# Optimization experiments

Measured on AMD Instinct MI355X. Metric: run time of the kernel, lower is better.

## Reference

```python
import jax, jax.numpy as jnp
from jax import lax
import numpy as np


def _conv(x, w, stride):
    # x: [B,C,D,H,W], w: [3,3,3,Cin,Cout]; kernel 3, pad 1 (matches SubMConv3d / SparseConv3d(3, s, padding=1))
    return lax.conv_general_dilated(x, w, (stride, stride, stride), [(1, 1)] * 3,
                                    dimension_numbers=('NCDHW', 'DHWIO', 'NCDHW'))


def _bn_relu(y, scale, shift, mask):
    # eval-mode BatchNorm folded to scale/shift, ReLU, then restrict to active sites
    return jnp.maximum(y * scale[None, :, None, None, None] + shift[None, :, None, None, None], 0.0) * mask


def _downsample_mask(m):
    # SparseConv3d(k=3, s=2, p=1): output site active iff any input in its 3x3x3 window is active
    return lax.reduce_window(m, -jnp.inf, lax.max, (1, 1, 3, 3, 3), (1, 1, 2, 2, 2),
                             [(0, 0), (0, 0), (1, 1), (1, 1), (1, 1)])


def setup_inputs() -> dict:
    key = jax.random.key(0)
    ks = jax.random.split(key, 40)
    B, D = 1, 128
    occ = jax.random.uniform(ks[0], (B, 1, D, D, D)) < 0.05
    x = jax.random.normal(ks[1], (B, 16, D, D, D), jnp.float32) * occ

    def w(k, ci, co):
        return jax.random.normal(k, (3, 3, 3, ci, co), jnp.float32) * (1.0 / np.sqrt(27.0 * ci))

    def sc(k, c):
        return jax.random.uniform(k, (c,), jnp.float32, 0.5, 1.5)

    def sh(k, c):
        return jax.random.normal(k, (c,), jnp.float32) * 0.1

    chans = [(16, 16), (16, 16), (16, 32), (32, 32), (32, 32), (32, 64), (64, 64), (64, 64), (64, 64)]
    names = ['w0a', 'w0b', 'wd0', 'w1a', 'w1b', 'wd1', 'w2a', 'w2b', 'w2c']
    d = {'x': x, 'mask': occ}
    i = 2
    for n, (ci, co) in zip(names, chans):
        d[n] = w(ks[i], ci, co)
        d['s' + n[1:]] = sc(ks[i + 1], co)
        d['b' + n[1:]] = sh(ks[i + 2], co)
        i += 3
    return d


def reference(x, mask, w0a, s0a, b0a, w0b, s0b, b0b, wd0, sd0, bd0,
              w1a, s1a, b1a, w1b, s1b, b1b, wd1, sd1, bd1,
              w2a, s2a, b2a, w2b, s2b, b2b, w2c, s2c, b2c):
    m0 = mask.astype(x.dtype)                       # active sites at full res [B,1,128,128,128]
    h = _bn_relu(_conv(x, w0a, 1), s0a, b0a, m0)    # conv0 (subm0)
    h = _bn_relu(_conv(h, w0b, 1), s0b, b0b, m0)
    m1 = _downsample_mask(m0)                       # down0 activity [B,1,64,64,64]
    h = _bn_relu(_conv(h, wd0, 2), sd0, bd0, m1)
    h = _bn_relu(_conv(h, w1a, 1), s1a, b1a, m1)    # conv1 (subm1)
    h = _bn_relu(_conv(h, w1b, 1), s1b, b1b, m1)
    m2 = _downsample_mask(m1)                       # down1 activity [B,1,32,32,32]
    h = _bn_relu(_conv(h, wd1, 2), sd1, bd1, m2)
    h = _bn_relu(_conv(h, w2a, 1), s2a, b2a, m2)    # conv2 (subm2)
    h = _bn_relu(_conv(h, w2b, 1), s2b, b2b, m2)
    h = _bn_relu(_conv(h, w2c, 1), s2c, b2c, m2)
    return h                                        # .dense() -> [B,64,32,32,32]
```

## Files before the change

### kernel.cpp

```cpp
#include <hip/hip_runtime.h>
#include <cstdint>

typedef unsigned short u16;
typedef unsigned int u32;
typedef unsigned char u8;
typedef unsigned long long u64;
typedef __attribute__((ext_vector_type(8))) short short8;
typedef __attribute__((ext_vector_type(4))) float f32x4;

#define CAP 131072

__device__ __forceinline__ float bf1(u16 v){ union{u32 i; float f;} c; c.i = ((u32)v) << 16; return c.f; }
__device__ __forceinline__ u16 f2bf(float f){
    union{float f; u32 i;} c; c.f = f; u32 i = c.i;
    return (u16)((i + 0x7FFFu + ((i >> 16) & 1u)) >> 16);
}
__device__ __forceinline__ u16 bits2bf(u32 b){ union{u32 i; float f;} c; c.i = b; return f2bf(c.f); }

struct PAll {
    const void* w[9];
    u32 wstart[10];
    int cin[9], cout[9], mode[9];
    const void* s[18];
};

__global__ __launch_bounds__(256)
void prepact_k(PAll J, u16* __restrict__ FR, float* __restrict__ S,
               const u16* __restrict__ s0a_probe, u32* __restrict__ flag,
               const void* __restrict__ xv, u64* __restrict__ bmask,
               u32* __restrict__ cnt, u16* __restrict__ Xp){
    int ok = 1;
    #pragma unroll
    for (int i = 0; i < 8; i += 2){
        u16 vv = s0a_probe[i];
        if (vv < 0x3F00u || vv > 0x3FC0u) ok = 0;
    }
    const u32 isbf = ok ? 1u : 0u;

    if (blockIdx.x < 8192){
        const int v = blockIdx.x * 256 + threadIdx.x;
        const size_t N = 2097152;
        u16 vals[16];
        u32 a = 0;
        if (isbf) {
            const u16* x = (const u16*)xv;
            #pragma unroll
            for (int c = 0; c < 16; ++c){
                const u16 b = x[(size_t)c * N + v];
                vals[c] = b;
                a |= (u32)b & 0x7FFFu;
            }
        } else {
            const u32* x = (const u32*)xv;
            #pragma unroll
            for (int c = 0; c < 16; ++c){
                const u32 b = x[(size_t)c * N + v];
                vals[c] = bits2bf(b);
                a |= b & 0x7FFFFFFFu;
            }
        }
        const bool act = (a != 0);
        const u64 m = __ballot(act);
        __shared__ u32 wc[4];
        const int lane = threadIdx.x & 63, wv = threadIdx.x >> 6;
        if (lane == 0) { bmask[v >> 6] = m; wc[wv] = (u32)__popcll(m); }
        __syncthreads();
        if (act){
            u32 wbase = 0;
            for (int i = 0; i < wv; ++i) wbase += wc[i];
            const u32 local = wbase + (u32)__popcll(m & ((1ull << lane) - 1ull));
            u16* dst = Xp + ((size_t)blockIdx.x * 256 + local) * 16;
            *(short8*)(dst)     = *(const short8*)(vals);
            *(short8*)(dst + 8) = *(const short8*)(vals + 8);
        }
        return;
    }

    const int gi = (int)(blockIdx.x - 8192) * 256 + threadIdx.x;
    if (gi == 0) { flag[0] = isbf; cnt[0] = 0; }

    const int wtot = (int)J.wstart[9];
    if (gi < wtot){
        int j = 0;
        while (gi >= (int)J.wstart[j + 1]) ++j;
        const int i = gi - (int)J.wstart[j];
        const void* w = J.w[j];
        const int CIN = J.cin[j], COUT = J.cout[j];
        const int jj = i & 7;
        const int lane = (i >> 3) & 63;
        int rest = i >> 9;
        int src = -1;
        if (J.mode[j] == 0){
            const int KC = CIN >> 5, NT = COUT >> 4;
            const int nt = rest % NT; rest /= NT;
            const int kc = rest % KC; const int tap = rest / KC;
            const int k = kc * 32 + (lane >> 4) * 8 + jj;
            const int co = nt * 16 + (lane & 15);
            src = (tap * CIN + k) * COUT + co;
        } else if (J.mode[j] == 1){
            const int nt = rest & 1; const int pair = rest >> 1;
            const int kg = (lane >> 4) * 8 + jj;
            const int tap = pair * 2 + (kg >> 4);
            const int ci = kg & 15;
            const int co = nt * 16 + (lane & 15);
            if (tap < 27) src = (tap * 16 + ci) * 32 + co;
        } else {
            const int pair = rest;
            const int kg = (lane >> 4) * 8 + jj;
            const int tap = pair * 2 + (kg >> 4);
            const int ci = kg & 15;
            const int co = lane & 15;
            if (tap < 27) src = (tap * 16 + ci) * 16 + co;
        }
        float v = 0.f;
        if (src >= 0) v = isbf ? bf1(((const u16*)w)[src]) : ((const float*)w)[src];
        FR[gi] = f2bf(v);
    } else {
        const int i2 = gi - wtot;
        const int len[18] = {16,16,16,16,32,32,32,32,32,32,64,64,64,64,64,64,64,64};
        const int off[18] = {0,16,32,48,64,96,128,160,192,224,256,320,384,448,512,576,640,704};
        if (i2 < 768){
            int b = 0, base = 0;
            while (i2 >= base + len[b]) { base += len[b]; ++b; }
            const int t = i2 - base;
            const float v = isbf ? bf1(((const u16*)J.s[b])[t]) : ((const float*)J.s[b])[t];
            S[off[b] + t] = v;
        }
    }
}

__global__ __launch_bounds__(256)
void scatter2m_k(const u16* __restrict__ Xp, const u64* __restrict__ bmask,
                 int* __restrict__ idxmap, int* __restrict__ alist,
                 u16* __restrict__ f, u32* __restrict__ cnt,
                 u8* __restrict__ m1, u8* __restrict__ m2){
    if (blockIdx.x < 512){
        const int lane = threadIdx.x & 63, wv = threadIdx.x >> 6;
        __shared__ u32 wcnt[16][4];
        __shared__ u32 tileoff[16];
        __shared__ u32 sbase;
        const int tile0 = blockIdx.x * 16;

        #pragma unroll
        for (int i = 0; i < 16; ++i){
            if (lane == 0){
                const u64 m = bmask[(size_t)(tile0 + i) * 4 + wv];
                wcnt[i][wv] = (u32)__popcll(m);
            }
        }
        __syncthreads();
        if (threadIdx.x == 0){
            u32 s = 0;
            #pragma unroll
            for (int i = 0; i < 16; ++i){
                tileoff[i] = s;
                s += wcnt[i][0] + wcnt[i][1] + wcnt[i][2] + wcnt[i][3];
            }
            sbase = atomicAdd(cnt, s);
        }
        __syncthreads();
        const u32 b0 = sbase;
        #pragma unroll
        for (int i = 0; i < 16; ++i){
            const u64 m = bmask[(size_t)(tile0 + i) * 4 + wv];
            const bool act = (m >> lane) & 1ull;
            u32 wbase = 0;
            for (int k = 0; k < wv; ++k) wbase += wcnt[i][k];
            const u32 rank = (u32)__popcll(m & ((1ull << lane) - 1ull));
            const int v = (tile0 + i) * 256 + threadIdx.x;
            int slot = -1;
            if (act){
                const u32 sl = b0 + tileoff[i] + wbase + rank;
                if (sl < CAP){
                    slot = (int)sl;
                    alist[slot] = v;
                    const u16* src = Xp + ((size_t)(tile0 + i) * 256 + wbase + rank) * 16;
                    u16* dst = f + (size_t)slot * 16;
                    *(short8*)(dst)     = *(const short8*)(src);
                    *(short8*)(dst + 8) = *(const short8*)(src + 8);
                }
            }
            idxmap[v] = slot;
        }
    } else if (blockIdx.x < 1536){
        const int v = (int)(blockIdx.x - 512) * 256 + threadIdx.x;
        const int xo = v & 63, yo = (v >> 6) & 63, zo = v >> 12;
        u32 a = 0;
        #pragma unroll
        for (int kz = 0; kz < 3; ++kz){ const int iz = 2*zo + kz - 1; if ((unsigned)iz >= 128u) continue;
          #pragma unroll
          for (int ky = 0; ky < 3; ++ky){ const int iy = 2*yo + ky - 1; if ((unsigned)iy >= 128u) continue;
            #pragma unroll
            for (int kx = 0; kx < 3; ++kx){ const int ix = 2*xo + kx - 1; if ((unsigned)ix >= 128u) continue;
              const int vv = (iz * 128 + iy) * 128 + ix;
              a |= (u32)((bmask[vv >> 6] >> (vv & 63)) & 1ull);
        }}}
        m1[v] = (u8)a;
    } else {
        const int v = (int)(blockIdx.x - 1536) * 256 + threadIdx.x;
        const int xo = v & 31, yo = (v >> 5) & 31, zo = v >> 10;
        const int xlo = max(0, 4*xo - 3), xhi = min(127, 4*xo + 3);
        const int w0 = xlo >> 6, w1 = xhi >> 6;
        u32 a = 0;
        #pragma unroll
        for (int dz = -3; dz <= 3; ++dz){ const int iz = 4*zo + dz; if ((unsigned)iz >= 128u) continue;
          #pragma unroll
          for (int dy = -3; dy <= 3; ++dy){ const int iy = 4*yo + dy; if ((unsigned)iy >= 128u) continue;
            const int rowword = ((iz * 128 + iy) * 128) >> 6;
            if (w0 == w1){
                const u64 mw = bmask[rowword + w0];
                const int sh = xlo & 63, len = xhi - xlo + 1;
                if ((mw >> sh) & ((1ull << len) - 1ull)) a = 1;
            } else {
                const u64 lo = bmask[rowword + w0] >> (xlo & 63);
                const u64 hi = bmask[rowword + w1] & ((1ull << ((xhi & 63) + 1)) - 1ull);
                if (lo | hi) a = 1;
            }
        }}
        m2[v] = (u8)a;
    }
}

__global__ __launch_bounds__(256)
void sconvm_k(const u16* __restrict__ fin, const int* __restrict__ idxmap,
              const int* __restrict__ alist, const u32* __restrict__ cnt,
              const u16* __restrict__ wf, const float* __restrict__ sc,
              const float* __restrict__ sh, u16* __restrict__ fout){
    const int n = min((int)cnt[0], CAP);
    const int j = blockIdx.x * 4 + (threadIdx.x >> 6);
    const int sbase = j * 16;
    if (sbase >= n) return;
    const int lane = threadIdx.x & 63;
    const int m = lane & 15, quad = lane >> 4;

    const int s = sbase + m;
    const int v = (s < n) ? alist[s] : -1;
    int xo = 0, yo = 0, zo = 0;
    if (v >= 0){ xo = v & 127; yo = (v >> 7) & 127; zo = v >> 14; }

    f32x4 acc = {0.f,0.f,0.f,0.f};
    #pragma unroll
    for (int p = 0; p < 14; ++p){
        const int tp = p * 2 + (quad >> 1);
        short8 a = {0,0,0,0,0,0,0,0};
        if (v >= 0 && tp < 27){
            const int kz = tp / 9, ky = (tp / 3) % 3, kx = tp % 3;
            const int iz = zo + kz - 1, iy = yo + ky - 1, ix = xo + kx - 1;
            if ((unsigned)iz < 128u && (unsigned)iy < 128u && (unsigned)ix < 128u){
                const int sn = idxmap[((size_t)iz * 128 + iy) * 128 + ix];
                if (sn >= 0) a = *(const short8*)(fin + (size_t)sn * 16 + (quad & 1) * 8);
            }
        }
        short8 b = *(const short8*)(wf + ((size_t)p * 64 + lane) * 8);
        acc = __builtin_amdgcn_mfma_f32_16x16x32_bf16(a, b, acc, 0, 0, 0);
    }

    const int co = lane & 15;
    const float scl = sc[co], shf = sh[co];
    #pragma unroll
    for (int r = 0; r < 4; ++r){
        const int srow = sbase + quad * 4 + r;
        if (srow < n){
            fout[(size_t)srow * 16 + co] = f2bf(fmaxf(acc[r] * scl + shf, 0.f));
        }
    }
}

__global__ __launch_bounds__(256)
void convd0m_k(const u16* __restrict__ fbuf, const int* __restrict__ idxmap,
               const u16* __restrict__ wf, const float* __restrict__ sc,
               const float* __restrict__ sh, const u8* __restrict__ mk,
               u16* __restrict__ out)
{
    const int wj = blockIdx.x * 4 + (threadIdx.x >> 6);
    const int lane = threadIdx.x & 63;
    const int m = lane & 15, quad = lane >> 4;
    const int xo_b = (wj & 3) * 16;
    const int yo = (wj >> 2) & 63;
    const int zo = wj >> 8;

    f32x4 acc0 = {0.f,0.f,0.f,0.f}, acc1 = {0.f,0.f,0.f,0.f};
    const int ix_m = (xo_b + m) * 2 - 1;

    #pragma unroll
    for (int p = 0; p < 14; ++p){
        const int tp = p * 2 + (quad >> 1);
        short8 a = {0,0,0,0,0,0,0,0};
        if (tp < 27){
            const int kz = tp / 9, ky = (tp / 3) % 3, kx = tp % 3;
            const int iz = 2*zo + kz - 1, iy = 2*yo + ky - 1, ix = ix_m + kx;
            if ((unsigned)iz < 128u && (unsigned)iy < 128u && (unsigned)ix < 128u){
                const int sn = idxmap[((size_t)iz * 128 + iy) * 128 + ix];
                if (sn >= 0) a = *(const short8*)(fbuf + (size_t)sn * 16 + (quad & 1) * 8);
            }
        }
        short8 b0 = *(const short8*)(wf + ((size_t)(p*2+0) * 64 + lane) * 8);
        short8 b1 = *(const short8*)(wf + ((size_t)(p*2+1) * 64 + lane) * 8);
        acc0 = __builtin_amdgcn_mfma_f32_16x16x32_bf16(a, b0, acc0, 0, 0, 0);
        acc1 = __builtin_amdgcn_mfma_f32_16x16x32_bf16(a, b1, acc1, 0, 0, 0);
    }

    const int vb = wj * 16 + quad * 4;
    const u32 m4 = *(const u32*)(mk + vb);
    const int n = lane & 15;
    #pragma unroll
    for (int nt = 0; nt < 2; ++nt){
        const int co = nt * 16 + n;
        const float s = sc[co], h = sh[co];
        const f32x4 acc = nt ? acc1 : acc0;
        #pragma unroll
        for (int r = 0; r < 4; ++r){
            float val = fmaxf(acc[r] * s + h, 0.f);
            val = ((m4 >> (8*r)) & 0xFFu) ? val : 0.f;
            out[(size_t)(vb + r) * 32 + co] = f2bf(val);
        }
    }
}

template<int DIN, int DOUT, int CIN, int COUT, int STRIDE, int NSPLIT, bool FINAL>
__global__ __launch_bounds__(256)
void mconv_k(const u16* __restrict__ in, const u16* __restrict__ wf,
             const float* __restrict__ sc, const float* __restrict__ sh,
             const u8* __restrict__ mk, void* __restrict__ out,
             const u32* __restrict__ flag)
{
    constexpr int KC = CIN / 32;
    constexpr int NT = COUT / 16;
    constexpr int NTE = NT / NSPLIT;
    constexpr int XT = DOUT / 16;
    const int wjj = blockIdx.x * 4 + (threadIdx.x >> 6);
    const int cs = wjj % NSPLIT;
    const int wj = wjj / NSPLIT;
    const int lane = threadIdx.x & 63;
    const int m = lane & 15, quad = lane >> 4;

    const int xo_b = (wj % XT) * 16;
    const int yo = (wj / XT) % DOUT;
    const int zo = wj / (XT * DOUT);

    f32x4 acc[NTE];
    #pragma unroll
    for (int i = 0; i < NTE; ++i) acc[i] = (f32x4){0.f,0.f,0.f,0.f};

    const int ix0 = (xo_b + m) * STRIDE - 1;
    for (int kz = 0; kz < 3; ++kz){
      const int iz = zo * STRIDE + kz - 1;
      if ((unsigned)iz >= (unsigned)DIN) continue;
      for (int ky = 0; ky < 3; ++ky){
        const int iy = yo * STRIDE + ky - 1;
        if ((unsigned)iy >= (unsigned)DIN) continue;
        const size_t rowb = ((size_t)iz * DIN + iy) * DIN;
        #pragma unroll
        for (int kx = 0; kx < 3; ++kx){
          const int ix = ix0 + kx;
          const bool v = (unsigned)ix < (unsigned)DIN;
          const int tap = (kz*3 + ky)*3 + kx;
          const u16* ap = in + (rowb + ix) * CIN + quad * 8;
          const u16* bp = wf + (size_t)tap * KC * NT * 512 + lane * 8;
          #pragma unroll
          for (int kc = 0; kc < KC; ++kc){
            short8 a = {0,0,0,0,0,0,0,0};
            if (v) a = *(const short8*)(ap + kc * 32);
            #pragma unroll
            for (int nt = 0; nt < NTE; ++nt){
              short8 b = *(const short8*)(bp + (kc * NT + cs * NTE + nt) * 512);
              acc[nt] = __builtin_amdgcn_mfma_f32_16x16x32_bf16(a, b, acc[nt], 0, 0, 0);
            }
          }
    }}}

    const int vb = wj * 16 + quad * 4;
    const u32 m4 = *(const u32*)(mk + vb);
    const int n = lane & 15;
    #pragma unroll
    for (int nt = 0; nt < NTE; ++nt){
        const int co = (cs * NTE + nt) * 16 + n;
        const float s = sc[co], h = sh[co];
        #pragma unroll
        for (int r = 0; r < 4; ++r){
            float val = fmaxf(acc[nt][r] * s + h, 0.f);
            val = ((m4 >> (8*r)) & 0xFFu) ? val : 0.f;
            ((u16*)out)[(size_t)(vb + r) * COUT + co] = f2bf(val);
        }
    }
    (void)flag;
}

template<int D, int CIN, int COUT, int CSPLIT, bool FINAL>
__global__ __launch_bounds__((D/32)*4*64*CSPLIT)
void mconvw_k(const u16* __restrict__ in, const u16* __restrict__ wf,
              const float* __restrict__ sc, const float* __restrict__ sh,
              const u8* __restrict__ mk, void* __restrict__ out,
              const u32* __restrict__ flag)
{
    constexpr int KC = CIN / 32;
    constexpr int NT = COUT / 16;
    constexpr int NTE = NT / CSPLIT;
    constexpr int CH8 = CIN / 8;
    constexpr int WPR = D / 32;
    constexpr int BT = WPR * 4 * 64 * CSPLIT;
    __shared__ u16 tile[16 * 2048];

    const int t = threadIdx.x;
    const int yp = blockIdx.x % (D / 2);
    const int zp = blockIdx.x / (D / 2);

    #pragma unroll
    for (int ri = 0; ri < 16; ++ri){
        const int dz = ri >> 2, jy = ri & 3;
        const int iz = 2*zp + dz - 1, iy = 2*yp + jy - 1;
        if ((unsigned)iz < (unsigned)D && (unsigned)iy < (unsigned)D){
            const u16* src = in + ((size_t)(iz * D + iy) * D) * CIN;
            u16* dst = &tile[ri * 2048];
            for (int c = t; c < D * CH8; c += BT){
                const int x = c / CH8, c8 = c % CH8;
                *(short8*)(dst + (c8 * D + x) * 8) = *(const short8*)(src + c * 8);
            }
        }
    }
    __syncthreads();

    const int lane = t & 63, w = t >> 6;
    const int cs = w % CSPLIT;
    const int w2 = w / CSPLIT;
    const int r = w2 / WPR;
    const int r2z = r >> 1, r2y = r & 1;
    const int xo_b = (w2 % WPR) * 32;
    const int zo = 2*zp + r2z, yo = 2*yp + r2y;
    const int m = lane & 15, quad = lane >> 4;

    f32x4 acc0[NTE], acc1[NTE];
    #pragma unroll
    for (int i = 0; i < NTE; ++i){ acc0[i] = (f32x4){0.f,0.f,0.f,0.f}; acc1[i] = (f32x4){0.f,0.f,0.f,0.f}; }

    #pragma unroll
    for (int kz = 0; kz < 3; ++kz){
      const int iz = zo + kz - 1;
      if ((unsigned)iz >= (unsigned)D) continue;
      #pragma unroll
      for (int ky = 0; ky < 3; ++ky){
        const int iy = yo + ky - 1;
        if ((unsigned)iy >= (unsigned)D) continue;
        const u16* row = &tile[((r2z + kz) * 4 + (r2y + ky)) * 2048];
        #pragma unroll
        for (int kx = 0; kx < 3; ++kx){
          const int ix0 = xo_b + m + kx - 1;
          const int ix1 = ix0 + 16;
          const bool aok0 = (unsigned)ix0 < (unsigned)D;
          const bool aok1 = (unsigned)ix1 < (unsigned)D;
          const int tap = (kz * 3 + ky) * 3 + kx;
          const u16* bp = wf + (size_t)tap * KC * NT * 512 + lane * 8;
          #pragma unroll
          for (int kc = 0; kc < KC; ++kc){
            short8 a0 = {0,0,0,0,0,0,0,0};
            short8 a1 = {0,0,0,0,0,0,0,0};
            if (aok0) a0 = *(const short8*)(row + ((kc * 4 + quad) * D + ix0) * 8);
            if (aok1) a1 = *(const short8*)(row + ((kc * 4 + quad) * D + ix1) * 8);
            #pragma unroll
            for (int nt = 0; nt < NTE; ++nt){
              short8 b = *(const short8*)(bp + (kc * NT + cs * NTE + nt) * 512);
              acc0[nt] = __builtin_amdgcn_mfma_f32_16x16x32_bf16(a0, b, acc0[nt], 0, 0, 0);
              acc1[nt] = __builtin_amdgcn_mfma_f32_16x16x32_bf16(a1, b, acc1[nt], 0, 0, 0);
            }
          }
        }
      }
    }

    const int base = (zo * D + yo) * D;
    const int vb0 = base + xo_b + quad * 4;
    const int vb1 = vb0 + 16;
    const u32 m4_0 = *(const u32*)(mk + vb0);
    const u32 m4_1 = *(const u32*)(mk + vb1);
    const int n = lane & 15;
    if (FINAL) {
        const bool bfout = flag[0] != 0;
        #pragma unroll
        for (int nt = 0; nt < NTE; ++nt){
            const int co = (cs * NTE + nt) * 16 + n;
            const float s = sc[co], h = sh[co];
            float4 o0, o1;
            float* p0 = &o0.x; float* p1 = &o1.x;
            #pragma unroll
            for (int r4 = 0; r4 < 4; ++r4){
                float v0 = fmaxf(acc0[nt][r4] * s + h, 0.f);
                float v1 = fmaxf(acc1[nt][r4] * s + h, 0.f);
                p0[r4] = ((m4_0 >> (8*r4)) & 0xFFu) ? v0 : 0.f;
                p1[r4] = ((m4_1 >> (8*r4)) & 0xFFu) ? v1 : 0.f;
            }
            if (!bfout) {
                *(float4*)((float*)out + (size_t)co * (D*D*D) + vb0) = o0;
                *(float4*)((float*)out + (size_t)co * (D*D*D) + vb1) = o1;
            } else {
                u16* ob0 = (u16*)out + (size_t)co * (D*D*D) + vb0;
                u16* ob1 = (u16*)out + (size_t)co * (D*D*D) + vb1;
                #pragma unroll
                for (int r4 = 0; r4 < 4; ++r4){ ob0[r4] = f2bf(p0[r4]); ob1[r4] = f2bf(p1[r4]); }
            }
        }
    } else {
        #pragma unroll
        for (int nt = 0; nt < NTE; ++nt){
            const int co = (cs * NTE + nt) * 16 + n;
            const float s = sc[co], h = sh[co];
            #pragma unroll
            for (int r4 = 0; r4 < 4; ++r4){
                float v0 = fmaxf(acc0[nt][r4] * s + h, 0.f);
                float v1 = fmaxf(acc1[nt][r4] * s + h, 0.f);
                v0 = ((m4_0 >> (8*r4)) & 0xFFu) ? v0 : 0.f;
                v1 = ((m4_1 >> (8*r4)) & 0xFFu) ? v1 : 0.f;
                ((u16*)out)[(size_t)(vb0 + r4) * COUT + co] = f2bf(v0);
                ((u16*)out)[(size_t)(vb1 + r4) * COUT + co] = f2bf(v1);
            }
        }
    }
}

extern "C" void kernel_launch(void* const* d_in, const int* in_sizes, int n_in,
                              void* d_out, int out_size, void* d_ws, size_t ws_size,
                              hipStream_t stream)
{
    (void)out_size; (void)ws_size;

    int wb = 2;
    for (int i = 1; i < n_in; ++i) { if (in_sizes[i] == 6912) { wb = i; break; } }

    const void* x = d_in[0];
    const void *w0a=d_in[wb+0],  *s0a=d_in[wb+1],  *b0a=d_in[wb+2];
    const void *w0b=d_in[wb+3],  *s0b=d_in[wb+4],  *b0b=d_in[wb+5];
    const void *wd0=d_in[wb+6],  *sd0=d_in[wb+7],  *bd0=d_in[wb+8];
    const void *w1a=d_in[wb+9],  *s1a=d_in[wb+10], *b1a=d_in[wb+11];
    const void *w1b=d_in[wb+12], *s1b=d_in[wb+13], *b1b=d_in[wb+14];
    const void *wd1=d_in[wb+15], *sd1=d_in[wb+16], *bd1=d_in[wb+17];
    const void *w2a=d_in[wb+18], *s2a=d_in[wb+19], *b2a=d_in[wb+20];
    const void *w2b=d_in[wb+21], *s2b=d_in[wb+22], *b2b=d_in[wb+23];
    const void *w2c=d_in[wb+24], *s2c=d_in[wb+25], *b2c=d_in[wb+26];

    char* ws = (char*)d_ws;
    int*   idxmap = (int*)(ws);
    u16*   Fb0    = (u16*)(ws + 8388608);
    u16*   Fb1    = (u16*)(ws + 12582912);
    u16*   Fb2    = (u16*)(ws + 16777216);
    u16*   Rb1    = (u16*)(ws + 25165824);
    u16*   Rb2    = (u16*)(ws + 41943040);
    u8*    m1     = (u8*)(ws + 58720256);
    u8*    m2     = (u8*)(ws + 58982400);
    u32*   cnt    = (u32*)(ws + 59015168);
    int*   alist  = (int*)(ws + 59015424);
    u16*   FR     = (u16*)(ws + 59539712);
    float* S      = (float*)(ws + 60483328);
    u32*   flag   = (u32*)(ws + 60486400);
    u64*   bmask  = (u64*)(ws + 60486656);
    u16*   Xp     = (u16*)(ws + 67108864);

    u16* wfs0a = FR + 0;
    u16* wfs0b = FR + 7168;
    u16* fd0   = FR + 14336;
    u16* f1a   = FR + 28672;
    u16* f1b   = FR + 56320;
    u16* fd1   = FR + 83968;
    u16* f2a   = FR + 139264;
    u16* f2b   = FR + 249856;
    u16* f2c   = FR + 360448;

    PAll J;
    const void* jsrc[9] = {w0a, w0b, wd0, w1a, w1b, wd1, w2a, w2b, w2c};
    const u32 jlen[9]   = {7168,7168,14336,27648,27648,55296,110592,110592,110592};
    const int jcin[9]   = {16,16,16,32,32,32,64,64,64};
    const int jcout[9]  = {16,16,32,32,32,64,64,64,64};
    const int jmode[9]  = {2,2,1,0,0,0,0,0,0};
    u32 acc = 0;
    for (int i = 0; i < 9; ++i){
        J.w[i] = jsrc[i]; J.wstart[i] = acc; acc += jlen[i];
        J.cin[i] = jcin[i]; J.cout[i] = jcout[i]; J.mode[i] = jmode[i];
    }
    J.wstart[9] = acc;
    const void* sv[18] = {s0a,b0a,s0b,b0b,sd0,bd0,s1a,b1a,s1b,b1b,sd1,bd1,s2a,b2a,s2b,b2b,s2c,b2c};
    for (int i = 0; i < 18; ++i) J.s[i] = sv[i];
    const u32 ptot = acc + 768;
    const int prep_blocks = (int)((ptot + 255) / 256);

    float *cs0a=S+0,  *cb0a=S+16,  *cs0b=S+32,  *cb0b=S+48;
    float *csd0=S+64, *cbd0=S+96,  *cs1a=S+128, *cb1a=S+160, *cs1b=S+192, *cb1b=S+224;
    float *csd1=S+256,*cbd1=S+320, *cs2a=S+384, *cb2a=S+448, *cs2b=S+512, *cb2b=S+576, *cs2c=S+640, *cb2c=S+704;

    prepact_k<<<8192 + prep_blocks, 256, 0, stream>>>(J, FR, S, (const u16*)s0a, flag,
                                                      x, bmask, cnt, Xp);
    scatter2m_k<<<1664, 256, 0, stream>>>(Xp, bmask, idxmap, alist, Fb0, cnt, m1, m2);

    sconvm_k<<<2048, 256, 0, stream>>>(Fb0, idxmap, alist, cnt, wfs0a, cs0a, cb0a, Fb1);
    sconvm_k<<<2048, 256, 0, stream>>>(Fb1, idxmap, alist, cnt, wfs0b, cs0b, cb0b, Fb2);
    convd0m_k<<<4096, 256, 0, stream>>>(Fb2, idxmap, fd0, csd0, cbd0, m1, Rb1);
    mconvw_k<64,32,32,1,false><<<1024, 512, 0, stream>>>(Rb1, f1a, cs1a, cb1a, m1, Rb2, flag);
    mconvw_k<64,32,32,1,false><<<1024, 512, 0, stream>>>(Rb2, f1b, cs1b, cb1b, m1, Rb1, flag);
    mconv_k<64,32,32,64,2,2,false><<<1024, 256, 0, stream>>>(Rb1, fd1, csd1, cbd1, m2, Rb2, flag);
    mconvw_k<32,64,64,2,false><<<256, 512, 0, stream>>>(Rb2, f2a, cs2a, cb2a, m2, Rb1, flag);
    mconvw_k<32,64,64,2,false><<<256, 512, 0, stream>>>(Rb1, f2b, cs2b, cb2b, m2, Rb2, flag);
    mconvw_k<32,64,64,2,true ><<<256, 512, 0, stream>>>(Rb2, f2c, cs2c, cb2c, m2, d_out, flag);
}
```

Baseline: 461.8 us.

## Fuse low-res tail convs into one cooperative kernel and prefetch sparse indices

Replaces the four launches at the 32^3 stage (downsample conv plus three submanifold-style convs) with one cooperative kernel of 256 blocks. Grid-wide syncs separate the stages, which removes per-launch overhead and inter-kernel gaps. The gather-based sparse convs now load all 14 index-map entries first, then do the feature gathers and MFMAs, so the index-load latency can overlap. Risks include the cost of the grid syncs, the cooperative launch needing all blocks co-resident (64KB shared memory per 512-thread block), and higher register pressure from the index array.

Result: slower. 762.5 us (+65.1%).

```diff
diff --git a/kernel.cpp b/kernel.cpp
--- a/kernel.cpp
+++ b/kernel.cpp
@@ -1,5 +1,8 @@
 #include <hip/hip_runtime.h>
+#include <hip/hip_cooperative_groups.h>
 #include <cstdint>
+
+namespace cg = cooperative_groups;
 
 typedef unsigned short u16;
 typedef unsigned int u32;
@@ -238,19 +241,26 @@
     int xo = 0, yo = 0, zo = 0;
     if (v >= 0){ xo = v & 127; yo = (v >> 7) & 127; zo = v >> 14; }
 
-    f32x4 acc = {0.f,0.f,0.f,0.f};
+    int sn[14];
     #pragma unroll
     for (int p = 0; p < 14; ++p){
         const int tp = p * 2 + (quad >> 1);
-        short8 a = {0,0,0,0,0,0,0,0};
+        int sv = -1;
         if (v >= 0 && tp < 27){
             const int kz = tp / 9, ky = (tp / 3) % 3, kx = tp % 3;
             const int iz = zo + kz - 1, iy = yo + ky - 1, ix = xo + kx - 1;
             if ((unsigned)iz < 128u && (unsigned)iy < 128u && (unsigned)ix < 128u){
-                const int sn = idxmap[((size_t)iz * 128 + iy) * 128 + ix];
-                if (sn >= 0) a = *(const short8*)(fin + (size_t)sn * 16 + (quad & 1) * 8);
-            }
-        }
+                sv = idxmap[((size_t)iz * 128 + iy) * 128 + ix];
+            }
+        }
+        sn[p] = sv;
+    }
+
+    f32x4 acc = {0.f,0.f,0.f,0.f};
+    #pragma unroll
+    for (int p = 0; p < 14; ++p){
+        short8 a = {0,0,0,0,0,0,0,0};
+        if (sn[p] >= 0) a = *(const short8*)(fin + (size_t)sn[p] * 16 + (quad & 1) * 8);
         short8 b = *(const short8*)(wf + ((size_t)p * 64 + lane) * 8);
         acc = __builtin_amdgcn_mfma_f32_16x16x32_bf16(a, b, acc, 0, 0, 0);
     }
@@ -278,22 +288,28 @@
     const int xo_b = (wj & 3) * 16;
     const int yo = (wj >> 2) & 63;
     const int zo = wj >> 8;
-
-    f32x4 acc0 = {0.f,0.f,0.f,0.f}, acc1 = {0.f,0.f,0.f,0.f};
     const int ix_m = (xo_b + m) * 2 - 1;
 
+    int sn[14];
     #pragma unroll
     for (int p = 0; p < 14; ++p){
         const int tp = p * 2 + (quad >> 1);
-        short8 a = {0,0,0,0,0,0,0,0};
+        int sv = -1;
         if (tp < 27){
             const int kz = tp / 9, ky = (tp / 3) % 3, kx = tp % 3;
             const int iz = 2*zo + kz - 1, iy = 2*yo + ky - 1, ix = ix_m + kx;
             if ((unsigned)iz < 128u && (unsigned)iy < 128u && (unsigned)ix < 128u){
-                const int sn = idxmap[((size_t)iz * 128 + iy) * 128 + ix];
-                if (sn >= 0) a = *(const short8*)(fbuf + (size_t)sn * 16 + (quad & 1) * 8);
-            }
-        }
+                sv = idxmap[((size_t)iz * 128 + iy) * 128 + ix];
+            }
+        }
+        sn[p] = sv;
+    }
+
+    f32x4 acc0 = {0.f,0.f,0.f,0.f}, acc1 = {0.f,0.f,0.f,0.f};
+    #pragma unroll
+    for (int p = 0; p < 14; ++p){
+        short8 a = {0,0,0,0,0,0,0,0};
+        if (sn[p] >= 0) a = *(const short8*)(fbuf + (size_t)sn[p] * 16 + (quad & 1) * 8);
         short8 b0 = *(const short8*)(wf + ((size_t)(p*2+0) * 64 + lane) * 8);
         short8 b1 = *(const short8*)(wf + ((size_t)(p*2+1) * 64 + lane) * 8);
         acc0 = __builtin_amdgcn_mfma_f32_16x16x32_bf16(a, b0, acc0, 0, 0, 0);
@@ -315,75 +331,6 @@
             out[(size_t)(vb + r) * 32 + co] = f2bf(val);
         }
     }
-}
-
-template<int DIN, int DOUT, int CIN, int COUT, int STRIDE, int NSPLIT, bool FINAL>
-__global__ __launch_bounds__(256)
-void mconv_k(const u16* __restrict__ in, const u16* __restrict__ wf,
-             const float* __restrict__ sc, const float* __restrict__ sh,
-             const u8* __restrict__ mk, void* __restrict__ out,
-             const u32* __restrict__ flag)
-{
-    constexpr int KC = CIN / 32;
-    constexpr int NT = COUT / 16;
-    constexpr int NTE = NT / NSPLIT;
-    constexpr int XT = DOUT / 16;
-    const int wjj = blockIdx.x * 4 + (threadIdx.x >> 6);
-    const int cs = wjj % NSPLIT;
-    const int wj = wjj / NSPLIT;
-    const int lane = threadIdx.x & 63;
-    const int m = lane & 15, quad = lane >> 4;
-
-    const int xo_b = (wj % XT) * 16;
-    const int yo = (wj / XT) % DOUT;
-    const int zo = wj / (XT * DOUT);
-
-    f32x4 acc[NTE];
-    #pragma unroll
-    for (int i = 0; i < NTE; ++i) acc[i] = (f32x4){0.f,0.f,0.f,0.f};
-
-    const int ix0 = (xo_b + m) * STRIDE - 1;
-    for (int kz = 0; kz < 3; ++kz){
-      const int iz = zo * STRIDE + kz - 1;
-      if ((unsigned)iz >= (unsigned)DIN) continue;
-      for (int ky = 0; ky < 3; ++ky){
-        const int iy = yo * STRIDE + ky - 1;
-        if ((unsigned)iy >= (unsigned)DIN) continue;
-        const size_t rowb = ((size_t)iz * DIN + iy) * DIN;
-        #pragma unroll
-        for (int kx = 0; kx < 3; ++kx){
-          const int ix = ix0 + kx;
-          const bool v = (unsigned)ix < (unsigned)DIN;
-          const int tap = (kz*3 + ky)*3 + kx;
-          const u16* ap = in + (rowb + ix) * CIN + quad * 8;
-          const u16* bp = wf + (size_t)tap * KC * NT * 512 + lane * 8;
-          #pragma unroll
-          for (int kc = 0; kc < KC; ++kc){
-            short8 a = {0,0,0,0,0,0,0,0};
-            if (v) a = *(const short8*)(ap + kc * 32);
-            #pragma unroll
-            for (int nt = 0; nt < NTE; ++nt){
-              short8 b = *(const short8*)(bp + (kc * NT + cs * NTE + nt) * 512);
-              acc[nt] = __builtin_amdgcn_mfma_f32_16x16x32_bf16(a, b, acc[nt], 0, 0, 0);
-            }
-          }
-    }}}
-
-    const int vb = wj * 16 + quad * 4;
-    const u32 m4 = *(const u32*)(mk + vb);
-    const int n = lane & 15;
-    #pragma unroll
-    for (int nt = 0; nt < NTE; ++nt){
-        const int co = (cs * NTE + nt) * 16 + n;
-        const float s = sc[co], h = sh[co];
-        #pragma unroll
-        for (int r = 0; r < 4; ++r){
-            float val = fmaxf(acc[nt][r] * s + h, 0.f);
-            val = ((m4 >> (8*r)) & 0xFFu) ? val : 0.f;
-            ((u16*)out)[(size_t)(vb + r) * COUT + co] = f2bf(val);
-        }
-    }
-    (void)flag;
 }
 
 template<int D, int CIN, int COUT, int CSPLIT, bool FINAL>
@@ -473,6 +420,166 @@
     const u32 m4_0 = *(const u32*)(mk + vb0);
     const u32 m4_1 = *(const u32*)(mk + vb1);
     const int n = lane & 15;
+    #pragma unroll
+    for (int nt = 0; nt < NTE; ++nt){
+        const int co = (cs * NTE + nt) * 16 + n;
+        const float s = sc[co], h = sh[co];
+        #pragma unroll
+        for (int r4 = 0; r4 < 4; ++r4){
+            float v0 = fmaxf(acc0[nt][r4] * s + h, 0.f);
+            float v1 = fmaxf(acc1[nt][r4] * s + h, 0.f);
+            v0 = ((m4_0 >> (8*r4)) & 0xFFu) ? v0 : 0.f;
+            v1 = ((m4_1 >> (8*r4)) & 0xFFu) ? v1 : 0.f;
+            ((u16*)out)[(size_t)(vb0 + r4) * COUT + co] = f2bf(v0);
+            ((u16*)out)[(size_t)(vb1 + r4) * COUT + co] = f2bf(v1);
+        }
+    }
+    (void)flag;
+}
+
+
+__device__ __forceinline__ void tail_d1(const u16* __restrict__ in, const u16* __restrict__ wf,
+                                        const float* __restrict__ sc, const float* __restrict__ sh,
+                                        const u8* __restrict__ mk, u16* __restrict__ out)
+{
+    const int w = threadIdx.x >> 6;
+    const int lane = threadIdx.x & 63;
+    const int m = lane & 15, quad = lane >> 4;
+    const int gw = blockIdx.x * 8 + w;
+
+    #pragma unroll
+    for (int ji = 0; ji < 2; ++ji){
+        const int wjj = gw * 2 + ji;
+        const int cs = wjj & 1;
+        const int wj = wjj >> 1;
+        const int xo_b = (wj & 1) * 16;
+        const int yo = (wj >> 1) & 31;
+        const int zo = wj >> 6;
+
+        f32x4 acc[2];
+        acc[0] = (f32x4){0.f,0.f,0.f,0.f};
+        acc[1] = (f32x4){0.f,0.f,0.f,0.f};
+
+        const int ix0 = (xo_b + m) * 2 - 1;
+        for (int kz = 0; kz < 3; ++kz){
+          const int iz = zo * 2 + kz - 1;
+          if ((unsigned)iz >= 64u) continue;
+          for (int ky = 0; ky < 3; ++ky){
+            const int iy = yo * 2 + ky - 1;
+            if ((unsigned)iy >= 64u) continue;
+            const size_t rowb = ((size_t)iz * 64 + iy) * 64;
+            #pragma unroll
+            for (int kx = 0; kx < 3; ++kx){
+              const int ix = ix0 + kx;
+              const bool vv = (unsigned)ix < 64u;
+              const int tap = (kz*3 + ky)*3 + kx;
+              const u16* ap = in + (rowb + ix) * 32 + quad * 8;
+              const u16* bp = wf + (size_t)tap * 4 * 512 + lane * 8;
+              short8 a = {0,0,0,0,0,0,0,0};
+              if (vv) a = *(const short8*)(ap);
+              #pragma unroll
+              for (int nt = 0; nt < 2; ++nt){
+                short8 b = *(const short8*)(bp + (cs * 2 + nt) * 512);
+                acc[nt] = __builtin_amdgcn_mfma_f32_16x16x32_bf16(a, b, acc[nt], 0, 0, 0);
+              }
+            }
+        }}
+
+        const int vb = wj * 16 + quad * 4;
+        const u32 m4 = *(const u32*)(mk + vb);
+        const int n = lane & 15;
+        #pragma unroll
+        for (int nt = 0; nt < 2; ++nt){
+            const int co = (cs * 2 + nt) * 16 + n;
+            const float s = sc[co], h = sh[co];
+            #pragma unroll
+            for (int r = 0; r < 4; ++r){
+                float val = fmaxf(acc[nt][r] * s + h, 0.f);
+                val = ((m4 >> (8*r)) & 0xFFu) ? val : 0.f;
+                out[(size_t)(vb + r) * 64 + co] = f2bf(val);
+            }
+        }
+    }
+}
+
+template<bool FINAL>
+__device__ __forceinline__ void tail_c32(u16* __restrict__ tile,
+                                         const u16* __restrict__ in, const u16* __restrict__ wf,
+                                         const float* __restrict__ sc, const float* __restrict__ sh,
+                                         const u8* __restrict__ mk, void* __restrict__ out,
+                                         const u32* __restrict__ flag)
+{
+    constexpr int D = 32, KC = 2, NT = 4, NTE = 2, CH8 = 8;
+    const int t = threadIdx.x;
+    const int yp = blockIdx.x % 16;
+    const int zp = blockIdx.x / 16;
+
+    #pragma unroll
+    for (int ri = 0; ri < 16; ++ri){
+        const int dz = ri >> 2, jy = ri & 3;
+        const int iz = 2*zp + dz - 1, iy = 2*yp + jy - 1;
+        if ((unsigned)iz < (unsigned)D && (unsigned)iy < (unsigned)D){
+            const u16* src = in + ((size_t)(iz * D + iy) * D) * 64;
+            u16* dst = &tile[ri * 2048];
+            for (int c = t; c < D * CH8; c += 512){
+                const int x = c / CH8, c8 = c % CH8;
+                *(short8*)(dst + (c8 * D + x) * 8) = *(const short8*)(src + c * 8);
+            }
+        }
+    }
+    __syncthreads();
+
+    const int lane = t & 63, w = t >> 6;
+    const int cs = w & 1;
+    const int w2 = w >> 1;
+    const int r2z = w2 >> 1, r2y = w2 & 1;
+    const int zo = 2*zp + r2z, yo = 2*yp + r2y;
+    const int m = lane & 15, quad = lane >> 4;
+
+    f32x4 acc0[NTE], acc1[NTE];
+    #pragma unroll
+    for (int i = 0; i < NTE; ++i){ acc0[i] = (f32x4){0.f,0.f,0.f,0.f}; acc1[i] = (f32x4){0.f,0.f,0.f,0.f}; }
+
+    #pragma unroll
+    for (int kz = 0; kz < 3; ++kz){
+      const int iz = zo + kz - 1;
+      if ((unsigned)iz >= (unsigned)D) continue;
+      #pragma unroll
+      for (int ky = 0; ky < 3; ++ky){
+        const int iy = yo + ky - 1;
+        if ((unsigned)iy >= (unsigned)D) continue;
+        const u16* row = &tile[((r2z + kz) * 4 + (r2y + ky)) * 2048];
+        #pragma unroll
+        for (int kx = 0; kx < 3; ++kx){
+          const int ix0 = m + kx - 1;
+          const int ix1 = ix0 + 16;
+          const bool aok0 = (unsigned)ix0 < (unsigned)D;
+          const bool aok1 = (unsigned)ix1 < (unsigned)D;
+          const int tap = (kz * 3 + ky) * 3 + kx;
+          const u16* bp = wf + (size_t)tap * KC * NT * 512 + lane * 8;
+          #pragma unroll
+          for (int kc = 0; kc < KC; ++kc){
+            short8 a0 = {0,0,0,0,0,0,0,0};
+            short8 a1 = {0,0,0,0,0,0,0,0};
+            if (aok0) a0 = *(const short8*)(row + ((kc * 4 + quad) * D + ix0) * 8);
+            if (aok1) a1 = *(const short8*)(row + ((kc * 4 + quad) * D + ix1) * 8);
+            #pragma unroll
+            for (int nt = 0; nt < NTE; ++nt){
+              short8 b = *(const short8*)(bp + (kc * NT + cs * NTE + nt) * 512);
+              acc0[nt] = __builtin_amdgcn_mfma_f32_16x16x32_bf16(a0, b, acc0[nt], 0, 0, 0);
+              acc1[nt] = __builtin_amdgcn_mfma_f32_16x16x32_bf16(a1, b, acc1[nt], 0, 0, 0);
+            }
+          }
+        }
+      }
+    }
+
+    const int base = (zo * D + yo) * D;
+    const int vb0 = base + quad * 4;
+    const int vb1 = vb0 + 16;
+    const u32 m4_0 = *(const u32*)(mk + vb0);
+    const u32 m4_1 = *(const u32*)(mk + vb1);
+    const int n = lane & 15;
     if (FINAL) {
         const bool bfout = flag[0] != 0;
         #pragma unroll
@@ -509,11 +616,33 @@
                 float v1 = fmaxf(acc1[nt][r4] * s + h, 0.f);
                 v0 = ((m4_0 >> (8*r4)) & 0xFFu) ? v0 : 0.f;
                 v1 = ((m4_1 >> (8*r4)) & 0xFFu) ? v1 : 0.f;
-                ((u16*)out)[(size_t)(vb0 + r4) * COUT + co] = f2bf(v0);
-                ((u16*)out)[(size_t)(vb1 + r4) * COUT + co] = f2bf(v1);
-            }
-        }
-    }
+                ((u16*)out)[(size_t)(vb0 + r4) * 64 + co] = f2bf(v0);
+                ((u16*)out)[(size_t)(vb1 + r4) * 64 + co] = f2bf(v1);
+            }
+        }
+    }
+}
+
+__global__ __launch_bounds__(512)
+void tail2_k(const u16* __restrict__ dn_in, u16* __restrict__ t0, u16* __restrict__ t1,
+             u16* __restrict__ t2, const u16* __restrict__ wd1f, const u16* __restrict__ w2af,
+             const u16* __restrict__ w2bf, const u16* __restrict__ w2cf,
+             const float* __restrict__ S, const u8* __restrict__ m2,
+             void* __restrict__ outp, const u32* __restrict__ flag)
+{
+    __shared__ u16 tile[16 * 2048];
+    cg::grid_group g = cg::this_grid();
+
+    tail_d1(dn_in, wd1f, S + 256, S + 320, m2, t0);
+    __threadfence();
+    g.sync();
+    tail_c32<false>(tile, t0, w2af, S + 384, S + 448, m2, t1, flag);
+    __threadfence();
+    g.sync();
+    tail_c32<false>(tile, t1, w2bf, S + 512, S + 576, m2, t2, flag);
+    __threadfence();
+    g.sync();
+    tail_c32<true >(tile, t2, w2cf, S + 640, S + 704, m2, outp, flag);
 }
 
 extern "C" void kernel_launch(void* const* d_in, const int* in_sizes, int n_in,
@@ -582,7 +711,6 @@
 
     float *cs0a=S+0,  *cb0a=S+16,  *cs0b=S+32,  *cb0b=S+48;
     float *csd0=S+64, *cbd0=S+96,  *cs1a=S+128, *cb1a=S+160, *cs1b=S+192, *cb1b=S+224;
-    float *csd1=S+256,*cbd1=S+320, *cs2a=S+384, *cb2a=S+448, *cs2b=S+512, *cb2b=S+576, *cs2c=S+640, *cb2c=S+704;
 
     prepact_k<<<8192 + prep_blocks, 256, 0, stream>>>(J, FR, S, (const u16*)s0a, flag,
                                                       x, bmask, cnt, Xp);
@@ -593,8 +721,11 @@
     convd0m_k<<<4096, 256, 0, stream>>>(Fb2, idxmap, fd0, csd0, cbd0, m1, Rb1);
     mconvw_k<64,32,32,1,false><<<1024, 512, 0, stream>>>(Rb1, f1a, cs1a, cb1a, m1, Rb2, flag);
     mconvw_k<64,32,32,1,false><<<1024, 512, 0, stream>>>(Rb2, f1b, cs1b, cb1b, m1, Rb1, flag);
-    mconv_k<64,32,32,64,2,2,false><<<1024, 256, 0, stream>>>(Rb1, fd1, csd1, cbd1, m2, Rb2, flag);
-    mconvw_k<32,64,64,2,false><<<256, 512, 0, stream>>>(Rb2, f2a, cs2a, cb2a, m2, Rb1, flag);
-    mconvw_k<32,64,64,2,false><<<256, 512, 0, stream>>>(Rb1, f2b, cs2b, cb2b, m2, Rb2, flag);
-    mconvw_k<32,64,64,2,true ><<<256, 512, 0, stream>>>(Rb2, f2c, cs2c, cb2c, m2, d_out, flag);
-}
+
+    const u16* a_dn = Rb1; u16* a_t0 = Rb2; u16* a_t1 = Fb0; u16* a_t2 = Fb1;
+    const u16* a_w0 = fd1; const u16* a_w1 = f2a; const u16* a_w2 = f2b; const u16* a_w3 = f2c;
+    const float* a_S = S; const u8* a_m2 = m2; void* a_out = d_out; const u32* a_flag = flag;
+    void* targs[12] = { &a_dn, &a_t0, &a_t1, &a_t2, &a_w0, &a_w1, &a_w2, &a_w3,
+                        &a_S, &a_m2, &a_out, &a_flag };
+    hipLaunchCooperativeKernel((void*)tail2_k, dim3(256), dim3(512), targs, 0, stream);
+}
```
